# Kernel optimization log

Hardware: AMD Instinct MI355X
Metric: run time of the kernel (lower is better)

## Reference

```python
import jax, jax.numpy as jnp
import numpy as np

HIDDEN = 1280
HEADS = 16
HEAD_DIM = HIDDEN // HEADS  # 80
B, N = 2, 2048


def _rotate_half(x):
    half = x.shape[-1] // 2
    return jnp.concatenate([-x[..., half:], x[..., :half]], axis=-1)


def setup_inputs() -> dict:
    key = jax.random.key(0)
    ks = jax.random.split(key, 7)
    x = jax.random.normal(ks[0], (B, N, HIDDEN), dtype=jnp.float32)
    cos = jax.random.uniform(ks[1], (N, HEAD_DIM), dtype=jnp.float32)
    sin = jax.random.uniform(ks[2], (N, HEAD_DIM), dtype=jnp.float32)
    s = 1.0 / np.sqrt(HIDDEN)
    qkv_w = jax.random.normal(ks[3], (HIDDEN, 3 * HIDDEN), dtype=jnp.float32) * s
    qkv_b = jax.random.normal(ks[4], (3 * HIDDEN,), dtype=jnp.float32) * 0.02
    proj_w = jax.random.normal(ks[5], (HIDDEN, HIDDEN), dtype=jnp.float32) * s
    proj_b = jax.random.normal(ks[6], (HIDDEN,), dtype=jnp.float32) * 0.02
    return {"x": x, "cos": cos, "sin": sin, "qkv_w": qkv_w, "qkv_b": qkv_b,
            "proj_w": proj_w, "proj_b": proj_b}


def reference(x, cos, sin, qkv_w, qkv_b, proj_w, proj_b):
    b, n, _ = x.shape
    scale = 1.0 / np.sqrt(HEAD_DIM).astype(np.float32)
    # fused QKV projection
    qkv = x @ qkv_w + qkv_b                                # [b, n, 3*hidden]
    qkv = qkv.reshape(b, n, 3, HEADS, HEAD_DIM)
    qkv = jnp.transpose(qkv, (2, 0, 3, 1, 4))              # [3, b, h, n, hd]
    q, k, v = qkv[0], qkv[1], qkv[2]
    # 2D RoPE
    cos_b = cos[None, None, :, :]
    sin_b = sin[None, None, :, :]
    q = q * cos_b + _rotate_half(q) * sin_b
    k = k * cos_b + _rotate_half(k) * sin_b
    # manual softmax attention
    scores = jnp.einsum('bhqd,bhkd->bhqk', q, k) * scale   # [b, h, n, n]
    attn = jax.nn.softmax(scores, axis=-1)
    out = jnp.einsum('bhqk,bhkd->bhqd', attn, v)           # [b, h, n, hd]
    out = jnp.transpose(out, (0, 2, 1, 3)).reshape(b, n, HIDDEN)
    return out @ proj_w + proj_b
```

## Files before the change

### kernel.cpp

```cpp
#include <hip/hip_runtime.h>
#include <hip/hip_bf16.h>
#include <math.h>

#define HIDDEN 1280
#define HEADS 16
#define HD 80
#define HALF 40
#define BB 2
#define NN 2048
#define MROWS (BB * NN)
#define QSCALE ((float)(0.11180339887498949 * 1.4426950408889634))

typedef __attribute__((ext_vector_type(8))) _Float16 f16x8;
typedef __attribute__((ext_vector_type(4))) float f32x4;

#define AS1 __attribute__((address_space(1)))
#define AS3 __attribute__((address_space(3)))

__device__ __forceinline__ void splitf16(float x, ushort& hi, ushort& lo) {
    _Float16 h = (_Float16)x;
    _Float16 l = (_Float16)(x - (float)h);
    hi = __builtin_bit_cast(ushort, h);
    lo = __builtin_bit_cast(ushort, l);
}

__device__ __forceinline__ ushort f2h(float x) {
    _Float16 h = (_Float16)x;
    return __builtin_bit_cast(ushort, h);
}

__global__ __launch_bounds__(256) void split_f16_kernel(
    const float* __restrict__ in, ushort* __restrict__ hi,
    ushort* __restrict__ lo, int n4)
{
    int i = blockIdx.x * 256 + threadIdx.x;
    if (i >= n4) return;
    float4 v = ((const float4*)in)[i];
    ushort4 h, l;
    splitf16(v.x, h.x, l.x);
    splitf16(v.y, h.y, l.y);
    splitf16(v.z, h.z, l.z);
    splitf16(v.w, h.w, l.w);
    ((ushort4*)hi)[i] = h;
    ((ushort4*)lo)[i] = l;
}

__global__ __launch_bounds__(256) void tsplit_f16_kernel(
    const float* __restrict__ W, ushort* __restrict__ T, int K, int N)
{
    __shared__ float s[32][33];
    const int n0 = blockIdx.x * 32;
    const int k0 = blockIdx.y * 32;
    {
        int tn = threadIdx.x & 31, tk = threadIdx.x >> 5;
        #pragma unroll
        for (int i = 0; i < 4; ++i)
            s[tk + i * 8][tn] = W[(size_t)(k0 + tk + i * 8) * N + n0 + tn];
    }
    __syncthreads();
    {
        int tk = threadIdx.x & 31, tn = threadIdx.x >> 5;
        #pragma unroll
        for (int i = 0; i < 4; ++i)
            T[(size_t)(n0 + tn + i * 8) * K + k0 + tk] = f2h(s[tk][tn + i * 8]);
    }
}

#define BM 128
#define BN 128
#define BK 32

__global__ __launch_bounds__(256) void gemm_f16x2_kernel(
    const ushort* __restrict__ Ahi, const ushort* __restrict__ Alo,
    const ushort* __restrict__ Bh,
    const float* __restrict__ bias, float* __restrict__ C,
    int M, int N, int K)
{
    __shared__ __align__(16) ushort lds[3 * 128 * 32];

    const int tid = threadIdx.x;
    const int wid = tid >> 6;
    const int lane = tid & 63;
    const int col0 = blockIdx.x * BN;
    const int row0 = blockIdx.y * BM;
    const int wy = wid >> 1, wx = wid & 1;
    const int lrow = lane >> 2;
    const int lchunk = lane & 3;

    f32x4 acc[4][4] = {};

    for (int k0 = 0; k0 < K; k0 += BK) {
        __syncthreads();
        #pragma unroll
        for (int i = 0; i < 6; ++i) {
            int s = wid + i * 4;
            int tile = s >> 3, t = s & 7;
            const ushort* src = (tile == 0) ? Ahi : (tile == 1) ? Alo : Bh;
            int srow = (tile < 2) ? row0 : col0;
            const ushort* g = src + (size_t)(srow + t * 16 + lrow) * K + k0 + lchunk * 8;
            ushort* l = lds + tile * 4096 + t * 512 + lane * 8;
            __builtin_amdgcn_global_load_lds(
                (const AS1 unsigned int*)g, (AS3 unsigned int*)l, 16, 0, 0);
        }
        __syncthreads();

        const int q = lane >> 4;
        const int r = lane & 15;
        f16x8 ah[4], al[4], bf[4];
        #pragma unroll
        for (int i = 0; i < 4; ++i) {
            int arow = wy * 64 + i * 16 + r;
            ah[i] = *(const f16x8*)(lds + 0 * 4096 + arow * 32 + q * 8);
            al[i] = *(const f16x8*)(lds + 1 * 4096 + arow * 32 + q * 8);
            int brow = wx * 64 + i * 16 + r;
            bf[i] = *(const f16x8*)(lds + 2 * 4096 + brow * 32 + q * 8);
        }
        #pragma unroll
        for (int i = 0; i < 4; ++i) {
            #pragma unroll
            for (int j = 0; j < 4; ++j) {
                acc[i][j] = __builtin_amdgcn_mfma_f32_16x16x32_f16(al[i], bf[j], acc[i][j], 0, 0, 0);
                acc[i][j] = __builtin_amdgcn_mfma_f32_16x16x32_f16(ah[i], bf[j], acc[i][j], 0, 0, 0);
            }
        }
    }

    const int q = lane >> 4, r = lane & 15;
    #pragma unroll
    for (int i = 0; i < 4; ++i) {
        #pragma unroll
        for (int j = 0; j < 4; ++j) {
            int col = col0 + wx * 64 + j * 16 + r;
            float b = bias[col];
            #pragma unroll
            for (int v = 0; v < 4; ++v) {
                int row = row0 + wy * 64 + i * 16 + q * 4 + v;
                C[(size_t)row * N + col] = acc[i][j][v] + b;
            }
        }
    }
}

__global__ __launch_bounds__(256) void rope_split_kernel(
    const float* __restrict__ qkv, const float* __restrict__ cos_t,
    const float* __restrict__ sin_t,
    ushort* __restrict__ qf, ushort* __restrict__ kf,
    ushort* __restrict__ vt)
{
    __shared__ float s_v[64][84];
    const int tid = threadIdx.x;
    const int b = blockIdx.z, h = blockIdx.y;
    const int n0 = blockIdx.x * 64;
    const int bh = b * HEADS + h;

    #pragma unroll
    for (int i = 0; i < 5; ++i) {
        int u = tid + i * 256;
        int n = u / 20, c = u % 20;
        const float* src = qkv + (size_t)(b * NN + n0 + n) * 3840 + 2 * HIDDEN + h * HD + c * 4;
        *(float4*)(&s_v[n][c * 4]) = *(const float4*)src;
    }

    for (int u = tid; u < 640; u += 256) {
        int n = u / 10, p = u % 10;
        int d = p * 4;
        int ng = n0 + n;
        size_t rowb = (size_t)(b * NN + ng) * 3840;
        float4 c0 = *(const float4*)(cos_t + ng * HD + d);
        float4 c1 = *(const float4*)(cos_t + ng * HD + d + HALF);
        float4 s0 = *(const float4*)(sin_t + ng * HD + d);
        float4 s1 = *(const float4*)(sin_t + ng * HD + d + HALF);
        size_t qo = ((size_t)bh * NN + ng) * 96;
        {
            float4 x0 = *(const float4*)(qkv + rowb + h * HD + d);
            float4 x1 = *(const float4*)(qkv + rowb + h * HD + d + HALF);
            ushort4 h4a, h4b;
            h4a.x = f2h((x0.x * c0.x - x1.x * s0.x) * QSCALE);
            h4a.y = f2h((x0.y * c0.y - x1.y * s0.y) * QSCALE);
            h4a.z = f2h((x0.z * c0.z - x1.z * s0.z) * QSCALE);
            h4a.w = f2h((x0.w * c0.w - x1.w * s0.w) * QSCALE);
            h4b.x = f2h((x1.x * c1.x + x0.x * s1.x) * QSCALE);
            h4b.y = f2h((x1.y * c1.y + x0.y * s1.y) * QSCALE);
            h4b.z = f2h((x1.z * c1.z + x0.z * s1.z) * QSCALE);
            h4b.w = f2h((x1.w * c1.w + x0.w * s1.w) * QSCALE);
            *(ushort4*)(qf + qo + d) = h4a;
            *(ushort4*)(qf + qo + d + HALF) = h4b;
        }
        {
            float4 x0 = *(const float4*)(qkv + rowb + HIDDEN + h * HD + d);
            float4 x1 = *(const float4*)(qkv + rowb + HIDDEN + h * HD + d + HALF);
            ushort4 h4a, h4b;
            h4a.x = f2h(x0.x * c0.x - x1.x * s0.x);
            h4a.y = f2h(x0.y * c0.y - x1.y * s0.y);
            h4a.z = f2h(x0.z * c0.z - x1.z * s0.z);
            h4a.w = f2h(x0.w * c0.w - x1.w * s0.w);
            h4b.x = f2h(x1.x * c1.x + x0.x * s1.x);
            h4b.y = f2h(x1.y * c1.y + x0.y * s1.y);
            h4b.z = f2h(x1.z * c1.z + x0.z * s1.z);
            h4b.w = f2h(x1.w * c1.w + x0.w * s1.w);
            *(ushort4*)(kf + qo + d) = h4a;
            *(ushort4*)(kf + qo + d + HALF) = h4b;
        }
    }

    {
        int which = tid >> 7;
        int u = tid & 127;
        int n = u >> 1, part = u & 1;
        size_t o = ((size_t)bh * NN + n0 + n) * 96 + 80 + part * 8;
        uint4 z = {0u, 0u, 0u, 0u};
        if (which == 0) *(uint4*)(qf + o) = z;
        else            *(uint4*)(kf + o) = z;
    }
    __syncthreads();

    for (int u = tid; u < 320; u += 256) {
        int d = u >> 2, nc = u & 3;
        ushort hs[16];
        #pragma unroll
        for (int kk = 0; kk < 16; ++kk)
            hs[kk] = f2h(s_v[nc * 16 + kk][d]);
        size_t o = ((size_t)bh * HD + d) * NN + n0 + nc * 16;
        uint4 w0, w1;
        w0.x = (uint)hs[0] | ((uint)hs[1] << 16);
        w0.y = (uint)hs[2] | ((uint)hs[3] << 16);
        w0.z = (uint)hs[4] | ((uint)hs[5] << 16);
        w0.w = (uint)hs[6] | ((uint)hs[7] << 16);
        w1.x = (uint)hs[8] | ((uint)hs[9] << 16);
        w1.y = (uint)hs[10] | ((uint)hs[11] << 16);
        w1.z = (uint)hs[12] | ((uint)hs[13] << 16);
        w1.w = (uint)hs[14] | ((uint)hs[15] << 16);
        *(uint4*)(vt + o) = w0;
        *(uint4*)(vt + o + 8) = w1;
    }
}

__global__ __launch_bounds__(256, 2) void attn_mfma_kernel(
    const ushort* __restrict__ qf, const ushort* __restrict__ kf,
    const ushort* __restrict__ vt,
    ushort* __restrict__ ao_hi, ushort* __restrict__ ao_lo)
{
    __shared__ __align__(16) ushort lds[20480];
    ushort* k_s = lds;
    _Float16* v_s = (_Float16*)(lds + 6144);
    _Float16* p_s = (_Float16*)(lds + 11264);

    const int tid = threadIdx.x;
    const int wave = tid >> 6, lane = tid & 63;
    const int quad = lane >> 4, r = lane & 15;
    const int b = blockIdx.z, h = blockIdx.y;
    const int bh = b * HEADS + h;
    const int q0 = blockIdx.x * 128;

    f16x8 qfr[2][3];
    #pragma unroll
    for (int mt = 0; mt < 2; ++mt)
        #pragma unroll
        for (int c = 0; c < 3; ++c) {
            size_t o = ((size_t)bh * NN + q0 + wave * 32 + mt * 16 + r) * 96 + c * 32 + quad * 8;
            qfr[mt][c] = *(const f16x8*)(qf + o);
        }

    f32x4 oacc[2][5] = {};
    float l_part[2][4] = {};

    const size_t kb = (size_t)bh * NN * 96;
    const size_t vb = (size_t)bh * HD * NN;

    for (int j0 = 0; j0 < NN; j0 += 64) {
        __syncthreads();
        for (int s = wave; s < 22; s += 4) {
            if (s < 12) {
                int off = s * 512 + lane * 8;
                __builtin_amdgcn_global_load_lds(
                    (const AS1 unsigned int*)(kf + kb + (size_t)j0 * 96 + off),
                    (AS3 unsigned int*)(k_s + off), 16, 0, 0);
            } else {
                int ts = s - 12;
                int off = ts * 512 + lane * 8;
                size_t go = vb + (size_t)(ts * 8 + (lane >> 3)) * NN + j0
                          + (size_t)(((lane & 7) ^ (lane >> 3)) * 8);
                __builtin_amdgcn_global_load_lds(
                    (const AS1 unsigned int*)(vt + go),
                    (AS3 unsigned int*)((ushort*)v_s + off), 16, 0, 0);
            }
        }
        __syncthreads();

        f32x4 sc[2][4] = {};
        #pragma unroll
        for (int jt = 0; jt < 4; ++jt) {
            f16x8 kbf[3];
            int j = jt * 16 + r;
            #pragma unroll
            for (int c = 0; c < 3; ++c)
                kbf[c] = *(const f16x8*)(k_s + j * 96 + c * 32 + quad * 8);
            #pragma unroll
            for (int mt = 0; mt < 2; ++mt)
                #pragma unroll
                for (int c = 0; c < 3; ++c)
                    sc[mt][jt] = __builtin_amdgcn_mfma_f32_16x16x32_f16(qfr[mt][c], kbf[c], sc[mt][jt], 0, 0, 0);
        }

        #pragma unroll
        for (int mt = 0; mt < 2; ++mt) {
            #pragma unroll
            for (int v = 0; v < 4; ++v) {
                float ps = 0.0f;
                #pragma unroll
                for (int jt = 0; jt < 4; ++jt) {
                    float p = __builtin_amdgcn_exp2f(sc[mt][jt][v]);
                    sc[mt][jt][v] = p;
                    ps += p;
                }
                l_part[mt][v] += ps;
            }
            int rowbase = wave * 32 + mt * 16 + quad * 4;
            #pragma unroll
            for (int jt = 0; jt < 4; ++jt) {
                int bks = (jt * 2 + (r >> 3)) ^ (quad << 1);
                #pragma unroll
                for (int v = 0; v < 4; ++v)
                    p_s[(rowbase + v) * 64 + bks * 8 + (r & 7)] = (_Float16)sc[mt][jt][v];
            }
        }

        f16x8 pa[2][2];
        #pragma unroll
        for (int mt = 0; mt < 2; ++mt)
            #pragma unroll
            for (int cc = 0; cc < 2; ++cc) {
                int rowp = wave * 32 + mt * 16 + r;
                int bks = (cc * 4 + quad) ^ (((r >> 2) & 3) << 1);
                pa[mt][cc] = *(const f16x8*)(p_s + rowp * 64 + bks * 8);
            }

        #pragma unroll
        for (int dt = 0; dt < 5; ++dt)
            #pragma unroll
            for (int cc = 0; cc < 2; ++cc) {
                int ck = (cc * 4 + quad) ^ (r & 7);
                f16x8 vbf = *(const f16x8*)(v_s + (dt * 16 + r) * 64 + ck * 8);
                oacc[0][dt] = __builtin_amdgcn_mfma_f32_16x16x32_f16(pa[0][cc], vbf, oacc[0][dt], 0, 0, 0);
                oacc[1][dt] = __builtin_amdgcn_mfma_f32_16x16x32_f16(pa[1][cc], vbf, oacc[1][dt], 0, 0, 0);
            }
    }

    float inv_l[2][4];
    #pragma unroll
    for (int mt = 0; mt < 2; ++mt)
        #pragma unroll
        for (int v = 0; v < 4; ++v) {
            float l = l_part[mt][v];
            l += __shfl_xor(l, 1);
            l += __shfl_xor(l, 2);
            l += __shfl_xor(l, 4);
            l += __shfl_xor(l, 8);
            inv_l[mt][v] = 1.0f / l;
        }

    __syncthreads();
    #pragma unroll
    for (int mt = 0; mt < 2; ++mt)
        #pragma unroll
        for (int v = 0; v < 4; ++v) {
            int row = wave * 32 + mt * 16 + quad * 4 + v;
            #pragma unroll
            for (int dt = 0; dt < 5; ++dt) {
                float o = oacc[mt][dt][v] * inv_l[mt][v];
                ushort hh, ll;
                splitf16(o, hh, ll);
                lds[row * 80 + dt * 16 + r] = hh;
                lds[10240 + row * 80 + dt * 16 + r] = ll;
            }
        }
    __syncthreads();
    {
        size_t gbase = ((size_t)b * NN + q0) * HIDDEN + h * HD;
        #pragma unroll
        for (int i = 0; i < 10; ++i) {
            int u = tid + i * 256;
            int plane = u / 1280, idx = u % 1280;
            int row = idx / 10, part = idx % 10;
            uint4 w = *(const uint4*)(lds + plane * 10240 + idx * 8);
            ushort* dst = (plane ? ao_lo : ao_hi) + gbase + (size_t)row * HIDDEN + part * 8;
            *(uint4*)dst = w;
        }
    }
}

extern "C" void kernel_launch(void* const* d_in, const int* in_sizes, int n_in,
                              void* d_out, int out_size, void* d_ws, size_t ws_size,
                              hipStream_t stream)
{
    const float* x      = (const float*)d_in[0];
    const float* cos_t  = (const float*)d_in[1];
    const float* sin_t  = (const float*)d_in[2];
    const float* qkv_w  = (const float*)d_in[3];
    const float* qkv_b  = (const float*)d_in[4];
    const float* proj_w = (const float*)d_in[5];
    const float* proj_b = (const float*)d_in[6];
    float* out = (float*)d_out;

    char* ws = (char*)d_ws;
    float*  qkv   = (float*)ws;
    ushort* ao_hi = (ushort*)ws;
    ushort* ao_lo = (ushort*)(ws + 10485760);
    ushort* wT    = (ushort*)(ws + 62914560);
    ushort* vt    = (ushort*)(ws + 62914560);
    ushort* a_hi  = (ushort*)(ws + 82575360);
    ushort* a_lo  = (ushort*)(ws + 93061120);
    ushort* q_f   = (ushort*)(ws + 83886080);
    ushort* k_f   = (ushort*)(ws + 96468992);

    split_f16_kernel<<<(MROWS * HIDDEN / 4 + 255) / 256, 256, 0, stream>>>(
        x, a_hi, a_lo, MROWS * HIDDEN / 4);

    tsplit_f16_kernel<<<dim3(3 * HIDDEN / 32, HIDDEN / 32), 256, 0, stream>>>(
        qkv_w, wT, HIDDEN, 3 * HIDDEN);

    gemm_f16x2_kernel<<<dim3(3 * HIDDEN / BN, MROWS / BM), 256, 0, stream>>>(
        a_hi, a_lo, wT, qkv_b, qkv, MROWS, 3 * HIDDEN, HIDDEN);

    rope_split_kernel<<<dim3(NN / 64, HEADS, BB), 256, 0, stream>>>(
        qkv, cos_t, sin_t, q_f, k_f, vt);

    attn_mfma_kernel<<<dim3(NN / 128, HEADS, BB), 256, 0, stream>>>(
        q_f, k_f, vt, ao_hi, ao_lo);

    tsplit_f16_kernel<<<dim3(HIDDEN / 32, HIDDEN / 32), 256, 0, stream>>>(
        proj_w, wT, HIDDEN, HIDDEN);

    gemm_f16x2_kernel<<<dim3(HIDDEN / BN, MROWS / BM), 256, 0, stream>>>(
        ao_hi, ao_lo, wT, proj_b, out, MROWS, HIDDEN, HIDDEN);
}
```

Baseline: 355.6 us.

## Add 256x256-tile triple-buffered split-f16 GEMM for QKV projection

Adds a new GEMM kernel with 512 threads and 256x256 output tiles for the QKV projection. It triple-buffers A-hi, A-lo and B tiles in LDS using direct global-to-LDS loads, and interleaves the prefetch with MFMA phases under barriers and setprio. It also remaps block IDs so consecutive blocks are spread across XCDs. The aim is more data reuse per tile and better hiding of load latency, at the cost of a large LDS footprint (144KB), heavy register use, and only 240 blocks, which may leave some CUs idle.

```diff
diff --git a/kernel.cpp b/kernel.cpp
--- a/kernel.cpp
+++ b/kernel.cpp
@@ -136,6 +136,191 @@
             for (int v = 0; v < 4; ++v) {
                 int row = row0 + wy * 64 + i * 16 + q * 4 + v;
                 C[(size_t)row * N + col] = acc[i][j][v] + b;
+            }
+        }
+    }
+}
+
+__global__ __launch_bounds__(512, 2) void gemm_f16x2_256_kernel(
+    const ushort* __restrict__ Ahi, const ushort* __restrict__ Alo,
+    const ushort* __restrict__ Bh,
+    const float* __restrict__ bias, float* __restrict__ C,
+    int M, int N, int K, int nbx)
+{
+    __shared__ __align__(16) ushort lds[3 * 3 * 8192];
+
+    const int tid = threadIdx.x;
+    const int wid = tid >> 6;
+    const int lane = tid & 63;
+    const int q = lane >> 4, r = lane & 15;
+    const int wr = wid >> 2, wc = wid & 3;
+
+    int id = blockIdx.x;
+    {
+        int nwg = gridDim.x;
+        if ((nwg & 7) == 0) {
+            int c = nwg >> 3;
+            id = (id & 7) * c + (id >> 3);
+        }
+    }
+    const int row0 = (id / nbx) * 256;
+    const int col0 = (id % nbx) * 256;
+
+    const ushort* gsrc[6];
+    int ldst[6];
+    #pragma unroll
+    for (int j = 0; j < 6; ++j) {
+        int pj = j >> 1;
+        int rloc = wid * 32 + (j & 1) * 16 + (lane >> 2);
+        int sl = (lane & 3) ^ ((rloc >> 1) & 3);
+        const ushort* base = (pj == 0) ? Ahi : (pj == 1) ? Alo : Bh;
+        int grow = ((pj < 2) ? row0 : col0) + rloc;
+        gsrc[j] = base + (size_t)grow * K + sl * 8;
+        ldst[j] = pj * 8192 + (wid * 32 + (j & 1) * 16) * 32 + lane * 8;
+    }
+
+    const int NT = K / 32;
+
+    #pragma unroll
+    for (int j = 0; j < 6; ++j)
+        __builtin_amdgcn_global_load_lds((const AS1 unsigned int*)(gsrc[j]),
+            (AS3 unsigned int*)(lds + ldst[j]), 16, 0, 0);
+    #pragma unroll
+    for (int j = 0; j < 6; ++j)
+        __builtin_amdgcn_global_load_lds((const AS1 unsigned int*)(gsrc[j] + 32),
+            (AS3 unsigned int*)(lds + 24576 + ldst[j]), 16, 0, 0);
+    asm volatile("s_waitcnt vmcnt(6)" ::: "memory");
+    __builtin_amdgcn_s_barrier();
+
+    const int soff = (q ^ ((r >> 1) & 3)) * 8;
+    const int arow0 = wr * 128 + r;
+    const int brow0 = wc * 64 + r;
+
+    f32x4 acc[8][4] = {};
+    f16x8 ah[4], al[4], bf[4];
+
+    int cb = 0;
+    int nb = 49152;
+
+    for (int t = 0; t < NT; ++t) {
+        const ushort* A0 = lds + cb;
+        const ushort* A1 = lds + cb + 8192;
+        const ushort* Bp = lds + cb + 16384;
+        ushort* nbuf = lds + nb;
+        const bool st = (t + 2 < NT);
+        const int ko = (t + 2) * 32;
+
+        #pragma unroll
+        for (int m = 0; m < 4; ++m) {
+            int ro = (arow0 + m * 16) * 32 + soff;
+            ah[m] = *(const f16x8*)(A0 + ro);
+            al[m] = *(const f16x8*)(A1 + ro);
+        }
+        #pragma unroll
+        for (int n = 0; n < 2; ++n)
+            bf[n] = *(const f16x8*)(Bp + (brow0 + n * 16) * 32 + soff);
+        if (st) {
+            __builtin_amdgcn_global_load_lds((const AS1 unsigned int*)(gsrc[0] + ko),
+                (AS3 unsigned int*)(nbuf + ldst[0]), 16, 0, 0);
+            __builtin_amdgcn_global_load_lds((const AS1 unsigned int*)(gsrc[1] + ko),
+                (AS3 unsigned int*)(nbuf + ldst[1]), 16, 0, 0);
+        }
+        __builtin_amdgcn_s_barrier();
+        asm volatile("s_waitcnt lgkmcnt(0)" ::: "memory");
+        __builtin_amdgcn_sched_barrier(0);
+        __builtin_amdgcn_s_setprio(1);
+        #pragma unroll
+        for (int m = 0; m < 4; ++m) {
+            #pragma unroll
+            for (int n = 0; n < 2; ++n) {
+                acc[m][n] = __builtin_amdgcn_mfma_f32_16x16x32_f16(al[m], bf[n], acc[m][n], 0, 0, 0);
+                acc[m][n] = __builtin_amdgcn_mfma_f32_16x16x32_f16(ah[m], bf[n], acc[m][n], 0, 0, 0);
+            }
+        }
+        __builtin_amdgcn_s_setprio(0);
+        __builtin_amdgcn_s_barrier();
+
+        #pragma unroll
+        for (int n = 2; n < 4; ++n)
+            bf[n] = *(const f16x8*)(Bp + (brow0 + n * 16) * 32 + soff);
+        if (st) {
+            __builtin_amdgcn_global_load_lds((const AS1 unsigned int*)(gsrc[2] + ko),
+                (AS3 unsigned int*)(nbuf + ldst[2]), 16, 0, 0);
+            __builtin_amdgcn_global_load_lds((const AS1 unsigned int*)(gsrc[3] + ko),
+                (AS3 unsigned int*)(nbuf + ldst[3]), 16, 0, 0);
+        }
+        __builtin_amdgcn_s_barrier();
+        asm volatile("s_waitcnt lgkmcnt(0)" ::: "memory");
+        __builtin_amdgcn_sched_barrier(0);
+        __builtin_amdgcn_s_setprio(1);
+        #pragma unroll
+        for (int m = 0; m < 4; ++m) {
+            #pragma unroll
+            for (int n = 2; n < 4; ++n) {
+                acc[m][n] = __builtin_amdgcn_mfma_f32_16x16x32_f16(al[m], bf[n], acc[m][n], 0, 0, 0);
+                acc[m][n] = __builtin_amdgcn_mfma_f32_16x16x32_f16(ah[m], bf[n], acc[m][n], 0, 0, 0);
+            }
+        }
+        __builtin_amdgcn_s_setprio(0);
+        __builtin_amdgcn_s_barrier();
+
+        #pragma unroll
+        for (int m = 0; m < 4; ++m) {
+            int ro = (arow0 + (m + 4) * 16) * 32 + soff;
+            ah[m] = *(const f16x8*)(A0 + ro);
+            al[m] = *(const f16x8*)(A1 + ro);
+        }
+        if (st) {
+            __builtin_amdgcn_global_load_lds((const AS1 unsigned int*)(gsrc[4] + ko),
+                (AS3 unsigned int*)(nbuf + ldst[4]), 16, 0, 0);
+            __builtin_amdgcn_global_load_lds((const AS1 unsigned int*)(gsrc[5] + ko),
+                (AS3 unsigned int*)(nbuf + ldst[5]), 16, 0, 0);
+        }
+        __builtin_amdgcn_s_barrier();
+        asm volatile("s_waitcnt lgkmcnt(0)" ::: "memory");
+        __builtin_amdgcn_sched_barrier(0);
+        __builtin_amdgcn_s_setprio(1);
+        #pragma unroll
+        for (int m = 0; m < 4; ++m) {
+            #pragma unroll
+            for (int n = 2; n < 4; ++n) {
+                acc[m + 4][n] = __builtin_amdgcn_mfma_f32_16x16x32_f16(al[m], bf[n], acc[m + 4][n], 0, 0, 0);
+                acc[m + 4][n] = __builtin_amdgcn_mfma_f32_16x16x32_f16(ah[m], bf[n], acc[m + 4][n], 0, 0, 0);
+            }
+        }
+        __builtin_amdgcn_s_setprio(0);
+        __builtin_amdgcn_s_barrier();
+
+        __builtin_amdgcn_s_setprio(1);
+        #pragma unroll
+        for (int m = 0; m < 4; ++m) {
+            #pragma unroll
+            for (int n = 0; n < 2; ++n) {
+                acc[m + 4][n] = __builtin_amdgcn_mfma_f32_16x16x32_f16(al[m], bf[n], acc[m + 4][n], 0, 0, 0);
+                acc[m + 4][n] = __builtin_amdgcn_mfma_f32_16x16x32_f16(ah[m], bf[n], acc[m + 4][n], 0, 0, 0);
+            }
+        }
+        __builtin_amdgcn_s_setprio(0);
+        if (st)
+            asm volatile("s_waitcnt vmcnt(6)" ::: "memory");
+        else if (t + 1 < NT)
+            asm volatile("s_waitcnt vmcnt(0)" ::: "memory");
+        __builtin_amdgcn_s_barrier();
+
+        cb += 24576; if (cb == 73728) cb = 0;
+        nb += 24576; if (nb == 73728) nb = 0;
+    }
+
+    #pragma unroll
+    for (int m = 0; m < 8; ++m) {
+        #pragma unroll
+        for (int n = 0; n < 4; ++n) {
+            int col = col0 + wc * 64 + n * 16 + r;
+            float b = bias[col];
+            #pragma unroll
+            for (int v = 0; v < 4; ++v) {
+                int row = row0 + wr * 128 + m * 16 + q * 4 + v;
+                C[(size_t)row * N + col] = acc[m][n][v] + b;
             }
         }
     }
@@ -419,8 +604,8 @@
     tsplit_f16_kernel<<<dim3(3 * HIDDEN / 32, HIDDEN / 32), 256, 0, stream>>>(
         qkv_w, wT, HIDDEN, 3 * HIDDEN);
 
-    gemm_f16x2_kernel<<<dim3(3 * HIDDEN / BN, MROWS / BM), 256, 0, stream>>>(
-        a_hi, a_lo, wT, qkv_b, qkv, MROWS, 3 * HIDDEN, HIDDEN);
+    gemm_f16x2_256_kernel<<<dim3((MROWS / 256) * (3 * HIDDEN / 256)), 512, 0, stream>>>(
+        a_hi, a_lo, wT, qkv_b, qkv, MROWS, 3 * HIDDEN, HIDDEN, 3 * HIDDEN / 256);
 
     rope_split_kernel<<<dim3(NN / 64, HEADS, BB), 256, 0, stream>>>(
         qkv, cos_t, sin_t, q_f, k_f, vt);
```

Result: faster. 324.7 us (-8.7%).
